# Optimization experiments

Measured on AMD Instinct MI355X. Metric: run time of the kernel, lower is better.

Reference implementation:

```python
import math
import jax, jax.numpy as jnp
import numpy as np

N_HEAD = 16
N_EMBD = 1024
HEAD_DIM = N_EMBD // N_HEAD  # 64
GROUP_SIZE = 64
RESIDUAL_LEN = 32
K_BITS = 2
V_BITS = 2
CLIP = 10000.0


def _fake_quant(x, mn, mx, bits):
    # asymmetric min-max quantize-dequantize with straight-through estimator
    qmax = float(2 ** bits - 1)
    scale = jnp.maximum((mx - mn) / qmax, 1e-8)
    q = jnp.round((x - mn) / scale)
    deq = q * scale + mn
    return x + jax.lax.stop_gradient(deq - x)


def quantize_key(k):
    # per-channel over token groups: [B,H,S,D] -> groups of GROUP_SIZE tokens,
    # min/max over the token axis within each group, per head_dim channel
    B, H, S, D = k.shape
    k = jnp.clip(k, -CLIP, CLIP)
    kg = k.reshape(B, H, S // GROUP_SIZE, GROUP_SIZE, D)
    mn = kg.min(axis=3, keepdims=True)
    mx = kg.max(axis=3, keepdims=True)
    return _fake_quant(kg, mn, mx, K_BITS).reshape(B, H, S, D)


def quantize_value(v):
    # per-token over channel groups: groups of GROUP_SIZE along head_dim
    B, H, S, D = v.shape
    g = GROUP_SIZE if (GROUP_SIZE > 0 and D % GROUP_SIZE == 0) else D
    v = jnp.clip(v, -CLIP, CLIP)
    vg = v.reshape(B, H, S, D // g, g)
    mn = vg.min(axis=-1, keepdims=True)
    mx = vg.max(axis=-1, keepdims=True)
    return _fake_quant(vg, mn, mx, V_BITS).reshape(B, H, S, D)


def setup_inputs() -> dict:
    key = jax.random.key(0)
    ks = jax.random.split(key, 5)
    B, S = 2, 2048
    scale_in = 1.0 / math.sqrt(N_EMBD)
    return {
        "x": jax.random.normal(ks[0], (B, S, N_EMBD), jnp.float32),
        "W_qkv": jax.random.normal(ks[1], (N_EMBD, 3 * N_EMBD), jnp.float32) * scale_in,
        "b_qkv": jax.random.normal(ks[2], (3 * N_EMBD,), jnp.float32) * 0.01,
        "W_proj": jax.random.normal(ks[3], (N_EMBD, N_EMBD), jnp.float32) * scale_in,
        "b_proj": jax.random.normal(ks[4], (N_EMBD,), jnp.float32) * 0.01,
    }


def reference(x, W_qkv, b_qkv, W_proj, b_proj):
    B, S, E = x.shape
    H, D = N_HEAD, HEAD_DIM
    qkv = x @ W_qkv + b_qkv                       # [B,S,3E]
    q, k, v = jnp.split(qkv, 3, axis=-1)
    split = lambda t: t.reshape(B, S, H, D).transpose(0, 2, 1, 3)  # [B,H,S,D]
    q, k, v = split(q), split(k), split(v)

    # KIVI: quantize all keys up to multiple of RESIDUAL_LEN, values except last RESIDUAL_LEN tokens
    if S > RESIDUAL_LEN:
        kql = (S // RESIDUAL_LEN) * RESIDUAL_LEN
        if kql > 0:
            k = jnp.concatenate([quantize_key(k[:, :, :kql]), k[:, :, kql:]], axis=2)
        vql = max(0, S - RESIDUAL_LEN)
        if vql > 0:
            v = jnp.concatenate([quantize_value(v[:, :, :vql]), v[:, :, vql:]], axis=2)

    attn = jnp.einsum("bhqd,bhkd->bhqk", q, k) / math.sqrt(D)
    if S > 1:
        mask = jnp.tril(jnp.ones((S, S), bool))
        attn = jnp.where(mask[None, None], attn, -jnp.inf)
    att = jax.nn.softmax(attn, axis=-1)
    y = jnp.einsum("bhqk,bhkd->bhqd", att, v)     # [B,H,S,D]
    y = y.transpose(0, 2, 1, 3).reshape(B, S, E)
    return y @ W_proj + b_proj
```

## Files before the change

### kernel.cpp

```cpp
#include <hip/hip_runtime.h>
#include <math.h>

#define BATCH 2
#define SEQ   2048
#define NHEAD 16
#define EMB   1024
#define N3E   3072
#define VQL   2016

typedef unsigned short ushort8_t __attribute__((ext_vector_type(8)));
typedef unsigned short ushort4_t __attribute__((ext_vector_type(4)));
typedef short bf16x8 __attribute__((ext_vector_type(8)));
typedef float f32x4 __attribute__((ext_vector_type(4)));
typedef unsigned int uint2_t __attribute__((ext_vector_type(2)));
typedef unsigned int uint4_t __attribute__((ext_vector_type(4)));

__device__ __forceinline__ float clipf(float x) {
    return fminf(fmaxf(x, -10000.0f), 10000.0f);
}
__device__ __forceinline__ float bf2f(unsigned short u) {
    return __uint_as_float(((unsigned)u) << 16);
}
__device__ __forceinline__ unsigned short f2bf(float f) {
    unsigned u = __float_as_uint(f);
    unsigned r = 0x7FFFu + ((u >> 16) & 1u);
    return (unsigned short)((u + r) >> 16);
}
__device__ __forceinline__ unsigned cvtpk(float lo, float hi) {
    unsigned r;
    asm("v_cvt_pk_bf16_f32 %0, %1, %2" : "=v"(r) : "v"(lo), "v"(hi));
    return r;
}

#define QK_PAD 40
__global__ __launch_bounds__(256, 2) void gemm_qkv_mfma(
    const float* __restrict__ X, const float* __restrict__ W,
    const float* __restrict__ bias,
    unsigned short* __restrict__ Qb, unsigned short* __restrict__ Kb,
    unsigned short* __restrict__ Vt)
{
    __shared__ unsigned short A3[3][128][QK_PAD];
    __shared__ unsigned short B3[3][128][QK_PAD];

    const int tid  = threadIdx.x;
    const int wave = tid >> 6, lane = tid & 63, lr = lane & 15, g = lane >> 4;
    const int wr = wave >> 1, wc = wave & 1;
    const int row0 = blockIdx.y * 128, col0 = blockIdx.x * 128;

    const int ra  = tid >> 1,        ca  = (tid & 1) * 16;
    const int cb4 = (tid & 31) * 4,  kb4 = (tid >> 5) * 4;

    const float* gA = X + (size_t)(row0 + ra) * 1024 + ca;
    const float* gB = W + (size_t)kb4 * N3E + col0 + cb4;

    float a_reg[16];
    float b_reg[4][4];

    #pragma unroll
    for (int i = 0; i < 4; ++i) *(float4*)&a_reg[i * 4] = *(const float4*)(gA + i * 4);
    #pragma unroll
    for (int i = 0; i < 4; ++i) *(float4*)b_reg[i] = *(const float4*)(gB + (size_t)i * N3E);

    f32x4 acc[4][4] = {};

    for (int t = 0; t < 32; ++t) {
        __syncthreads();
        unsigned pw[3][8];
        #pragma unroll
        for (int p = 0; p < 8; ++p) {
            float x0 = a_reg[2 * p], x1 = a_reg[2 * p + 1];
            unsigned h = cvtpk(x0, x1);
            float h0 = __uint_as_float(h << 16), h1 = __uint_as_float(h & 0xFFFF0000u);
            float r0 = x0 - h0, r1 = x1 - h1;
            unsigned m = cvtpk(r0, r1);
            float m0 = __uint_as_float(m << 16), m1 = __uint_as_float(m & 0xFFFF0000u);
            unsigned l = cvtpk(r0 - m0, r1 - m1);
            pw[0][p] = h; pw[1][p] = m; pw[2][p] = l;
        }
        #pragma unroll
        for (int term = 0; term < 3; ++term) {
            *(uint4_t*)&A3[term][ra][ca]     = *(uint4_t*)&pw[term][0];
            *(uint4_t*)&A3[term][ra][ca + 8] = *(uint4_t*)&pw[term][4];
        }
        #pragma unroll
        for (int j = 0; j < 4; ++j) {
            unsigned wh[2], wm[2], wl[2];
            #pragma unroll
            for (int ii = 0; ii < 2; ++ii) {
                float x0 = b_reg[2 * ii][j], x1 = b_reg[2 * ii + 1][j];
                unsigned h = cvtpk(x0, x1);
                float h0 = __uint_as_float(h << 16), h1 = __uint_as_float(h & 0xFFFF0000u);
                float r0 = x0 - h0, r1 = x1 - h1;
                unsigned m = cvtpk(r0, r1);
                float m0 = __uint_as_float(m << 16), m1 = __uint_as_float(m & 0xFFFF0000u);
                unsigned l = cvtpk(r0 - m0, r1 - m1);
                wh[ii] = h; wm[ii] = m; wl[ii] = l;
            }
            *(uint2_t*)&B3[0][cb4 + j][kb4] = *(uint2_t*)wh;
            *(uint2_t*)&B3[1][cb4 + j][kb4] = *(uint2_t*)wm;
            *(uint2_t*)&B3[2][cb4 + j][kb4] = *(uint2_t*)wl;
        }
        __syncthreads();

        if (t < 31) {
            #pragma unroll
            for (int i = 0; i < 4; ++i)
                *(float4*)&a_reg[i * 4] = *(const float4*)(gA + (t + 1) * 32 + i * 4);
            #pragma unroll
            for (int i = 0; i < 4; ++i)
                *(float4*)b_reg[i] = *(const float4*)(gB + (size_t)((t + 1) * 32 + i) * N3E);
        }

        bf16x8 af[3][4];
        #pragma unroll
        for (int term = 0; term < 3; ++term)
            #pragma unroll
            for (int m = 0; m < 4; ++m)
                af[term][m] = *(const bf16x8*)&A3[term][wr * 64 + m * 16 + lr][g * 8];
        #pragma unroll
        for (int n = 0; n < 4; ++n) {
            bf16x8 bh = *(const bf16x8*)&B3[0][wc * 64 + n * 16 + lr][g * 8];
            bf16x8 bm = *(const bf16x8*)&B3[1][wc * 64 + n * 16 + lr][g * 8];
            bf16x8 bl = *(const bf16x8*)&B3[2][wc * 64 + n * 16 + lr][g * 8];
            #pragma unroll
            for (int m = 0; m < 4; ++m)
                acc[m][n] = __builtin_amdgcn_mfma_f32_16x16x32_bf16(af[0][m], bh, acc[m][n], 0, 0, 0);
            #pragma unroll
            for (int m = 0; m < 4; ++m)
                acc[m][n] = __builtin_amdgcn_mfma_f32_16x16x32_bf16(af[0][m], bm, acc[m][n], 0, 0, 0);
            #pragma unroll
            for (int m = 0; m < 4; ++m)
                acc[m][n] = __builtin_amdgcn_mfma_f32_16x16x32_bf16(af[1][m], bh, acc[m][n], 0, 0, 0);
            #pragma unroll
            for (int m = 0; m < 4; ++m)
                acc[m][n] = __builtin_amdgcn_mfma_f32_16x16x32_bf16(af[1][m], bm, acc[m][n], 0, 0, 0);
            #pragma unroll
            for (int m = 0; m < 4; ++m)
                acc[m][n] = __builtin_amdgcn_mfma_f32_16x16x32_bf16(af[0][m], bl, acc[m][n], 0, 0, 0);
            #pragma unroll
            for (int m = 0; m < 4; ++m)
                acc[m][n] = __builtin_amdgcn_mfma_f32_16x16x32_bf16(af[2][m], bh, acc[m][n], 0, 0, 0);
        }
    }

    const int which = col0 >> 10;
    const int hcol  = ((col0 + wc * 64) & 1023) >> 6;
    const int b     = row0 >> 11;
    const int s_base = (row0 & 2047) + wr * 64;

    float bo[4];
    #pragma unroll
    for (int n = 0; n < 4; ++n) bo[n] = bias[col0 + wc * 64 + n * 16 + lr];
    #pragma unroll
    for (int m = 0; m < 4; ++m)
        #pragma unroll
        for (int n = 0; n < 4; ++n)
            #pragma unroll
            for (int r = 0; r < 4; ++r)
                acc[m][n][r] += bo[n];

    if (which == 0) {
        unsigned short* qdst = Qb + (((size_t)b * NHEAD + hcol) * SEQ) * 64;
        #pragma unroll
        for (int m = 0; m < 4; ++m)
            #pragma unroll
            for (int r = 0; r < 4; ++r) {
                int s = s_base + m * 16 + g * 4 + r;
                #pragma unroll
                for (int n = 0; n < 4; ++n)
                    qdst[(size_t)s * 64 + n * 16 + lr] = f2bf(acc[m][n][r]);
            }
    } else if (which == 1) {
        #pragma unroll
        for (int n = 0; n < 4; ++n) {
            float cmn = INFINITY, cmx = -INFINITY;
            #pragma unroll
            for (int m = 0; m < 4; ++m)
                #pragma unroll
                for (int r = 0; r < 4; ++r) {
                    float v = clipf(acc[m][n][r]);
                    acc[m][n][r] = v;
                    cmn = fminf(cmn, v); cmx = fmaxf(cmx, v);
                }
            cmn = fminf(cmn, __shfl_xor(cmn, 16)); cmx = fmaxf(cmx, __shfl_xor(cmx, 16));
            cmn = fminf(cmn, __shfl_xor(cmn, 32)); cmx = fmaxf(cmx, __shfl_xor(cmx, 32));
            float scale = fmaxf((cmx - cmn) / 3.0f, 1e-8f);
            #pragma unroll
            for (int m = 0; m < 4; ++m)
                #pragma unroll
                for (int r = 0; r < 4; ++r)
                    acc[m][n][r] = rintf((acc[m][n][r] - cmn) / scale) * scale + cmn;
        }
        unsigned short* kdst = Kb + (((size_t)b * NHEAD + hcol) * SEQ) * 64;
        #pragma unroll
        for (int m = 0; m < 4; ++m)
            #pragma unroll
            for (int r = 0; r < 4; ++r) {
                int s = s_base + m * 16 + g * 4 + r;
                #pragma unroll
                for (int n = 0; n < 4; ++n)
                    kdst[(size_t)s * 64 + n * 16 + lr] = f2bf(acc[m][n][r]);
            }
    } else {
        #pragma unroll
        for (int m = 0; m < 4; ++m)
            #pragma unroll
            for (int r = 0; r < 4; ++r) {
                float c[4];
                #pragma unroll
                for (int n = 0; n < 4; ++n) c[n] = clipf(acc[m][n][r]);
                float mn = fminf(fminf(c[0], c[1]), fminf(c[2], c[3]));
                float mx = fmaxf(fmaxf(c[0], c[1]), fmaxf(c[2], c[3]));
                #pragma unroll
                for (int msk = 1; msk < 16; msk <<= 1) {
                    mn = fminf(mn, __shfl_xor(mn, msk));
                    mx = fmaxf(mx, __shfl_xor(mx, msk));
                }
                int s = s_base + m * 16 + g * 4 + r;
                if (s < VQL) {
                    float scale = fmaxf((mx - mn) / 3.0f, 1e-8f);
                    #pragma unroll
                    for (int n = 0; n < 4; ++n)
                        acc[m][n][r] = rintf((c[n] - mn) / scale) * scale + mn;
                }
            }
        #pragma unroll
        for (int m = 0; m < 4; ++m)
            #pragma unroll
            for (int n = 0; n < 4; ++n) {
                ushort4_t o;
                #pragma unroll
                for (int r = 0; r < 4; ++r) o[r] = f2bf(acc[m][n][r]);
                *(ushort4_t*)(Vt + ((((size_t)b * NHEAD + hcol) * 64) + n * 16 + lr) * SEQ
                                 + s_base + m * 16 + g * 4) = o;
            }
    }
}

__global__ __launch_bounds__(256) void attn_mfma(
    unsigned short* __restrict__ QY,
    const unsigned short* __restrict__ K,
    const unsigned short* __restrict__ Vt)
{
    __shared__ unsigned short Ks [64][72];
    __shared__ unsigned short VsT[64][72];
    __shared__ unsigned short Ps [4][16][72];

    const int tid  = threadIdx.x;
    const int wave = tid >> 6;
    const int lane = tid & 63;
    const int lr   = lane & 15;
    const int g    = lane >> 4;

    const int bid = blockIdx.x;
    const int qt  = 31 - (bid >> 5);
    const int bh  = bid & 31;
    const size_t base = (size_t)bh * (SEQ * 64);

    const int qrow = qt * 64 + wave * 16 + lr;
    const unsigned short* qp = QY + base + (size_t)qrow * 64;
    bf16x8 aq[2];
    #pragma unroll
    for (int ka = 0; ka < 2; ++ka)
        aq[ka] = *(const bf16x8*)(qp + ka * 32 + g * 8);

    f32x4 o[4] = {};
    float m[4]    = {-1e30f, -1e30f, -1e30f, -1e30f};
    float lsum[4] = {};
    const float sc = 0.125f;

    const int str = tid >> 2;
    const int stc = (tid & 3) << 4;

    for (int jt = 0; jt <= qt; ++jt) {
        __syncthreads();
        {
            const unsigned short* kg = K + base + ((size_t)(jt * 64 + str) << 6) + stc;
            *(ushort8_t*)&Ks[str][stc]     = *(const ushort8_t*)kg;
            *(ushort8_t*)&Ks[str][stc + 8] = *(const ushort8_t*)(kg + 8);
            const unsigned short* vg = Vt + base + ((size_t)str << 11) + jt * 64 + stc;
            *(ushort8_t*)&VsT[str][stc]     = *(const ushort8_t*)vg;
            *(ushort8_t*)&VsT[str][stc + 8] = *(const ushort8_t*)(vg + 8);
        }
        __syncthreads();

        f32x4 s[4] = {};
        #pragma unroll
        for (int f = 0; f < 4; ++f) {
            #pragma unroll
            for (int ka = 0; ka < 2; ++ka) {
                bf16x8 bk = *(const bf16x8*)&Ks[f * 16 + lr][ka * 32 + g * 8];
                s[f] = __builtin_amdgcn_mfma_f32_16x16x32_bf16(aq[ka], bk, s[f], 0, 0, 0);
            }
        }

        const bool diag = (jt == qt);
        float mx[4];
        #pragma unroll
        for (int r = 0; r < 4; ++r) {
            const int ql = wave * 16 + g * 4 + r;
            float vmax = -1e30f;
            #pragma unroll
            for (int f = 0; f < 4; ++f) {
                float v = s[f][r] * sc;
                if (diag && (f * 16 + lr) > ql) v = -1e30f;
                s[f][r] = v;
                vmax = fmaxf(vmax, v);
            }
            mx[r] = vmax;
        }
        #pragma unroll
        for (int msk = 1; msk < 16; msk <<= 1)
            #pragma unroll
            for (int r = 0; r < 4; ++r)
                mx[r] = fmaxf(mx[r], __shfl_xor(mx[r], msk));

        float alpha[4], tsum[4];
        #pragma unroll
        for (int r = 0; r < 4; ++r) {
            float mn = fmaxf(m[r], mx[r]);
            alpha[r] = __expf(m[r] - mn);
            m[r] = mn;
            float ts = 0.0f;
            #pragma unroll
            for (int f = 0; f < 4; ++f) {
                float p = __expf(s[f][r] - mn);
                unsigned short ub = f2bf(p);
                Ps[wave][g * 4 + r][f * 16 + lr] = ub;
                ts += bf2f(ub);
            }
            tsum[r] = ts;
        }
        #pragma unroll
        for (int msk = 1; msk < 16; msk <<= 1)
            #pragma unroll
            for (int r = 0; r < 4; ++r)
                tsum[r] += __shfl_xor(tsum[r], msk);
        #pragma unroll
        for (int r = 0; r < 4; ++r) {
            lsum[r] = lsum[r] * alpha[r] + tsum[r];
            #pragma unroll
            for (int df = 0; df < 4; ++df) o[df][r] *= alpha[r];
        }

        asm volatile("s_waitcnt lgkmcnt(0)" ::: "memory");
        __builtin_amdgcn_sched_barrier(0);

        bf16x8 pa[2];
        #pragma unroll
        for (int kb = 0; kb < 2; ++kb)
            pa[kb] = *(const bf16x8*)&Ps[wave][lr][kb * 32 + g * 8];
        #pragma unroll
        for (int df = 0; df < 4; ++df) {
            #pragma unroll
            for (int kb = 0; kb < 2; ++kb) {
                bf16x8 vb = *(const bf16x8*)&VsT[df * 16 + lr][kb * 32 + g * 8];
                o[df] = __builtin_amdgcn_mfma_f32_16x16x32_bf16(pa[kb], vb, o[df], 0, 0, 0);
            }
        }
    }

    float invl[4];
    #pragma unroll
    for (int r = 0; r < 4; ++r) invl[r] = 1.0f / lsum[r];
    #pragma unroll
    for (int df = 0; df < 4; ++df)
        #pragma unroll
        for (int r = 0; r < 4; ++r) {
            int q = qt * 64 + wave * 16 + g * 4 + r;
            QY[base + (size_t)q * 64 + df * 16 + lr] = f2bf(o[df][r] * invl[r]);
        }
}

#define PJ_PAD 72
__global__ __launch_bounds__(256, 2) void gemm_proj_mfma(
    const unsigned short* __restrict__ Y, const float* __restrict__ W,
    const float* __restrict__ bias, float* __restrict__ C)
{
    __shared__ unsigned short A2[2][128][PJ_PAD];
    __shared__ unsigned short B2[2][128][PJ_PAD];

    const int tid  = threadIdx.x;
    const int wave = tid >> 6, lane = tid & 63, lr = lane & 15, g = lane >> 4;
    const int wr = wave >> 1, wc = wave & 1;
    const int row0 = blockIdx.y * 128, col0 = blockIdx.x * 128;
    const int b = row0 >> 11, s0 = row0 & 2047;

    const int ra  = tid >> 1,       ca  = (tid & 1) * 32;
    const int cb4 = (tid & 31) * 4, kb4 = (tid >> 5) * 4;

    ushort8_t a_reg[4];
    float bw[2][4][4];

    {
        const unsigned short* gy = Y + ((((size_t)b * NHEAD + 0) * SEQ + s0 + ra) << 6) + ca;
        #pragma unroll
        for (int i = 0; i < 4; ++i) a_reg[i] = *(const ushort8_t*)(gy + i * 8);
        const float* gw = W + (size_t)kb4 * EMB + col0 + cb4;
        #pragma unroll
        for (int half = 0; half < 2; ++half)
            #pragma unroll
            for (int i = 0; i < 4; ++i)
                *(float4*)bw[half][i] = *(const float4*)(gw + (size_t)(half * 32 + i) * EMB);
        #pragma unroll
        for (int i = 0; i < 4; ++i) *(ushort8_t*)&A2[0][ra][ca + i * 8] = a_reg[i];
        #pragma unroll
        for (int half = 0; half < 2; ++half)
            #pragma unroll
            for (int j = 0; j < 4; ++j) {
                unsigned w2[2];
                w2[0] = cvtpk(bw[half][0][j], bw[half][1][j]);
                w2[1] = cvtpk(bw[half][2][j], bw[half][3][j]);
                *(uint2_t*)&B2[0][cb4 + j][half * 32 + kb4] = *(uint2_t*)w2;
            }
    }
    __syncthreads();

    f32x4 acc[4][4] = {};

    for (int t = 0; t < 16; ++t) {
        const int cur = t & 1;
        if (t < 15) {
            const unsigned short* gy =
                Y + ((((size_t)b * NHEAD + (t + 1)) * SEQ + s0 + ra) << 6) + ca;
            #pragma unroll
            for (int i = 0; i < 4; ++i) a_reg[i] = *(const ushort8_t*)(gy + i * 8);
            const float* gw = W + (size_t)((t + 1) * 64 + kb4) * EMB + col0 + cb4;
            #pragma unroll
            for (int half = 0; half < 2; ++half)
                #pragma unroll
                for (int i = 0; i < 4; ++i)
                    *(float4*)bw[half][i] = *(const float4*)(gw + (size_t)(half * 32 + i) * EMB);
        }
        #pragma unroll
        for (int kk = 0; kk < 2; ++kk) {
            bf16x8 af[4];
            #pragma unroll
            for (int m = 0; m < 4; ++m)
                af[m] = *(const bf16x8*)&A2[cur][wr * 64 + m * 16 + lr][kk * 32 + g * 8];
            #pragma unroll
            for (int n = 0; n < 4; ++n) {
                bf16x8 bf = *(const bf16x8*)&B2[cur][wc * 64 + n * 16 + lr][kk * 32 + g * 8];
                #pragma unroll
                for (int m = 0; m < 4; ++m)
                    acc[m][n] = __builtin_amdgcn_mfma_f32_16x16x32_bf16(af[m], bf, acc[m][n], 0, 0, 0);
            }
        }
        if (t < 15) {
            const int nxt = cur ^ 1;
            #pragma unroll
            for (int i = 0; i < 4; ++i) *(ushort8_t*)&A2[nxt][ra][ca + i * 8] = a_reg[i];
            #pragma unroll
            for (int half = 0; half < 2; ++half)
                #pragma unroll
                for (int j = 0; j < 4; ++j) {
                    unsigned w2[2];
                    w2[0] = cvtpk(bw[half][0][j], bw[half][1][j]);
                    w2[1] = cvtpk(bw[half][2][j], bw[half][3][j]);
                    *(uint2_t*)&B2[nxt][cb4 + j][half * 32 + kb4] = *(uint2_t*)w2;
                }
        }
        __syncthreads();
    }

    float bo[4];
    #pragma unroll
    for (int n = 0; n < 4; ++n) bo[n] = bias[col0 + wc * 64 + n * 16 + lr];
    #pragma unroll
    for (int m = 0; m < 4; ++m)
        #pragma unroll
        for (int r = 0; r < 4; ++r) {
            int mrow = row0 + wr * 64 + m * 16 + g * 4 + r;
            #pragma unroll
            for (int n = 0; n < 4; ++n)
                C[(size_t)mrow * EMB + col0 + wc * 64 + n * 16 + lr] = acc[m][n][r] + bo[n];
        }
}

extern "C" void kernel_launch(void* const* d_in, const int* in_sizes, int n_in,
                              void* d_out, int out_size, void* d_ws, size_t ws_size,
                              hipStream_t stream)
{
    const float* x     = (const float*)d_in[0];
    const float* Wqkv  = (const float*)d_in[1];
    const float* bqkv  = (const float*)d_in[2];
    const float* Wproj = (const float*)d_in[3];
    const float* bproj = (const float*)d_in[4];
    float* out = (float*)d_out;

    const size_t QKV_ELEMS = (size_t)BATCH * NHEAD * SEQ * 64;
    unsigned short* q  = (unsigned short*)d_ws;
    unsigned short* kb = q + QKV_ELEMS;
    unsigned short* vt = kb + QKV_ELEMS;

    gemm_qkv_mfma<<<dim3(N3E / 128, 4096 / 128), 256, 0, stream>>>(x, Wqkv, bqkv, q, kb, vt);
    attn_mfma<<<dim3(32 * 32), 256, 0, stream>>>(q, kb, vt);
    gemm_proj_mfma<<<dim3(EMB / 128, 4096 / 128), 256, 0, stream>>>(q, Wproj, bproj, out);
}
```

Baseline: 310.4 us.

## Pre-split QKV operands to bf16 and repair near-tie quantization values

The fused in-loop fp32-to-3xbf16 splitting in the QKV GEMM is replaced by separate pre-pass kernels that split X into two bf16 terms and transposed W into three. The GEMM then runs three bf16 product passes (hh, hm, mh) instead of six, loading tiles with async global-to-LDS copies into swizzled shared memory. Because the reduced precision can flip K/V quantization rounding near half-integer boundaries, near-tie elements are recorded through an atomic counter. A repair kernel recomputes those elements in higher precision. The cost is extra kernels, workspace traffic, and atomics, and the repair list is capped at a fixed size.

```diff
diff --git a/kernel.cpp b/kernel.cpp
--- a/kernel.cpp
+++ b/kernel.cpp
@@ -7,13 +7,15 @@
 #define EMB   1024
 #define N3E   3072
 #define VQL   2016
+#define REC_CAP 65536
 
 typedef unsigned short ushort8_t __attribute__((ext_vector_type(8)));
 typedef unsigned short ushort4_t __attribute__((ext_vector_type(4)));
 typedef short bf16x8 __attribute__((ext_vector_type(8)));
 typedef float f32x4 __attribute__((ext_vector_type(4)));
 typedef unsigned int uint2_t __attribute__((ext_vector_type(2)));
-typedef unsigned int uint4_t __attribute__((ext_vector_type(4)));
+
+struct __align__(16) Rec { unsigned dst; unsigned mn_pack; float mn; float scale; };
 
 __device__ __forceinline__ float clipf(float x) {
     return fminf(fmaxf(x, -10000.0f), 10000.0f);
@@ -31,115 +33,132 @@
     asm("v_cvt_pk_bf16_f32 %0, %1, %2" : "=v"(r) : "v"(lo), "v"(hi));
     return r;
 }
-
-#define QK_PAD 40
-__global__ __launch_bounds__(256, 2) void gemm_qkv_mfma(
-    const float* __restrict__ X, const float* __restrict__ W,
+__device__ __forceinline__ void async_copy16(const unsigned short* g, unsigned short* lds) {
+    __builtin_amdgcn_global_load_lds(
+        (const __attribute__((address_space(1))) unsigned int*)g,
+        (__attribute__((address_space(3))) unsigned int*)lds, 16, 0, 0);
+}
+
+__global__ __launch_bounds__(256) void split_x_kernel(
+    const float* __restrict__ X,
+    unsigned short* __restrict__ Xh, unsigned short* __restrict__ Xm)
+{
+    const size_t i8 = ((size_t)blockIdx.x * 256 + threadIdx.x) * 8;
+    float4 a = *(const float4*)(X + i8);
+    float4 b = *(const float4*)(X + i8 + 4);
+    float xs[8] = {a.x, a.y, a.z, a.w, b.x, b.y, b.z, b.w};
+    ushort8_t h8, m8;
+    #pragma unroll
+    for (int j = 0; j < 8; ++j) {
+        unsigned short h = f2bf(xs[j]);
+        h8[j] = h;
+        m8[j] = f2bf(xs[j] - bf2f(h));
+    }
+    *(ushort8_t*)(Xh + i8) = h8;
+    *(ushort8_t*)(Xm + i8) = m8;
+}
+
+__global__ __launch_bounds__(256) void split_wt_kernel(
+    const float* __restrict__ W,
+    unsigned short* __restrict__ WTh, unsigned short* __restrict__ WTm,
+    unsigned short* __restrict__ WTl)
+{
+    __shared__ float t[64][65];
+    const int tid = threadIdx.x;
+    const int nt = blockIdx.x * 64, kt = blockIdx.y * 64;
+    const int r = tid >> 2, cg = (tid & 3) * 16;
+    #pragma unroll
+    for (int j = 0; j < 4; ++j) {
+        float4 v = *(const float4*)(W + (size_t)(kt + r) * N3E + nt + cg + j * 4);
+        t[r][cg + j * 4 + 0] = v.x; t[r][cg + j * 4 + 1] = v.y;
+        t[r][cg + j * 4 + 2] = v.z; t[r][cg + j * 4 + 3] = v.w;
+    }
+    __syncthreads();
+    ushort8_t h8[2], m8[2], l8[2];
+    #pragma unroll
+    for (int j = 0; j < 16; ++j) {
+        float v = t[cg + j][r];
+        unsigned short h = f2bf(v);
+        float r1 = v - bf2f(h);
+        unsigned short mm = f2bf(r1);
+        float r2 = r1 - bf2f(mm);
+        h8[j >> 3][j & 7] = h; m8[j >> 3][j & 7] = mm; l8[j >> 3][j & 7] = f2bf(r2);
+    }
+    size_t off = (size_t)(nt + r) * 1024 + kt + cg;
+    *(ushort8_t*)(WTh + off) = h8[0]; *(ushort8_t*)(WTh + off + 8) = h8[1];
+    *(ushort8_t*)(WTm + off) = m8[0]; *(ushort8_t*)(WTm + off + 8) = m8[1];
+    *(ushort8_t*)(WTl + off) = l8[0]; *(ushort8_t*)(WTl + off + 8) = l8[1];
+}
+
+__global__ void zero_cnt_kernel(unsigned* c) {
+    if (threadIdx.x == 0 && blockIdx.x == 0) *c = 0;
+}
+
+__device__ __forceinline__ void push_flag(unsigned* cnt, Rec* recs, unsigned dst,
+                                          int mg, int ng, float mn, float scale) {
+    unsigned idx = atomicAdd(cnt, 1u);
+    if (idx < REC_CAP) {
+        Rec r; r.dst = dst; r.mn_pack = (unsigned)mg | ((unsigned)ng << 12);
+        r.mn = mn; r.scale = scale;
+        recs[idx] = r;
+    }
+}
+
+__global__ __launch_bounds__(256) void gemm_qkv3(
+    const unsigned short* __restrict__ Xh, const unsigned short* __restrict__ Xm,
+    const unsigned short* __restrict__ WTh, const unsigned short* __restrict__ WTm,
     const float* __restrict__ bias,
     unsigned short* __restrict__ Qb, unsigned short* __restrict__ Kb,
-    unsigned short* __restrict__ Vt)
-{
-    __shared__ unsigned short A3[3][128][QK_PAD];
-    __shared__ unsigned short B3[3][128][QK_PAD];
+    unsigned short* __restrict__ Vt,
+    unsigned* __restrict__ cnt, Rec* __restrict__ recs)
+{
+    __shared__ __align__(16) unsigned short As[128 * 64];
+    __shared__ __align__(16) unsigned short Bs[128 * 64];
 
     const int tid  = threadIdx.x;
     const int wave = tid >> 6, lane = tid & 63, lr = lane & 15, g = lane >> 4;
     const int wr = wave >> 1, wc = wave & 1;
     const int row0 = blockIdx.y * 128, col0 = blockIdx.x * 128;
-
-    const int ra  = tid >> 1,        ca  = (tid & 1) * 16;
-    const int cb4 = (tid & 31) * 4,  kb4 = (tid >> 5) * 4;
-
-    const float* gA = X + (size_t)(row0 + ra) * 1024 + ca;
-    const float* gB = W + (size_t)kb4 * N3E + col0 + cb4;
-
-    float a_reg[16];
-    float b_reg[4][4];
-
-    #pragma unroll
-    for (int i = 0; i < 4; ++i) *(float4*)&a_reg[i * 4] = *(const float4*)(gA + i * 4);
-    #pragma unroll
-    for (int i = 0; i < 4; ++i) *(float4*)b_reg[i] = *(const float4*)(gB + (size_t)i * N3E);
+    const int lr7 = lr & 7;
+
+    const int drow = lane >> 3;
+    const int swz8 = ((lane & 7) ^ drow) * 8;
+    const int arow0 = wave * 32;
+
+    const unsigned short* Aseg[3] = {Xh, Xh, Xm};
+    const unsigned short* Bseg[3] = {WTh, WTm, WTh};
 
     f32x4 acc[4][4] = {};
 
-    for (int t = 0; t < 32; ++t) {
-        __syncthreads();
-        unsigned pw[3][8];
-        #pragma unroll
-        for (int p = 0; p < 8; ++p) {
-            float x0 = a_reg[2 * p], x1 = a_reg[2 * p + 1];
-            unsigned h = cvtpk(x0, x1);
-            float h0 = __uint_as_float(h << 16), h1 = __uint_as_float(h & 0xFFFF0000u);
-            float r0 = x0 - h0, r1 = x1 - h1;
-            unsigned m = cvtpk(r0, r1);
-            float m0 = __uint_as_float(m << 16), m1 = __uint_as_float(m & 0xFFFF0000u);
-            unsigned l = cvtpk(r0 - m0, r1 - m1);
-            pw[0][p] = h; pw[1][p] = m; pw[2][p] = l;
-        }
-        #pragma unroll
-        for (int term = 0; term < 3; ++term) {
-            *(uint4_t*)&A3[term][ra][ca]     = *(uint4_t*)&pw[term][0];
-            *(uint4_t*)&A3[term][ra][ca + 8] = *(uint4_t*)&pw[term][4];
-        }
-        #pragma unroll
-        for (int j = 0; j < 4; ++j) {
-            unsigned wh[2], wm[2], wl[2];
-            #pragma unroll
-            for (int ii = 0; ii < 2; ++ii) {
-                float x0 = b_reg[2 * ii][j], x1 = b_reg[2 * ii + 1][j];
-                unsigned h = cvtpk(x0, x1);
-                float h0 = __uint_as_float(h << 16), h1 = __uint_as_float(h & 0xFFFF0000u);
-                float r0 = x0 - h0, r1 = x1 - h1;
-                unsigned m = cvtpk(r0, r1);
-                float m0 = __uint_as_float(m << 16), m1 = __uint_as_float(m & 0xFFFF0000u);
-                unsigned l = cvtpk(r0 - m0, r1 - m1);
-                wh[ii] = h; wm[ii] = m; wl[ii] = l;
-            }
-            *(uint2_t*)&B3[0][cb4 + j][kb4] = *(uint2_t*)wh;
-            *(uint2_t*)&B3[1][cb4 + j][kb4] = *(uint2_t*)wm;
-            *(uint2_t*)&B3[2][cb4 + j][kb4] = *(uint2_t*)wl;
-        }
-        __syncthreads();
-
-        if (t < 31) {
-            #pragma unroll
-            for (int i = 0; i < 4; ++i)
-                *(float4*)&a_reg[i * 4] = *(const float4*)(gA + (t + 1) * 32 + i * 4);
-            #pragma unroll
-            for (int i = 0; i < 4; ++i)
-                *(float4*)b_reg[i] = *(const float4*)(gB + (size_t)((t + 1) * 32 + i) * N3E);
-        }
-
-        bf16x8 af[3][4];
-        #pragma unroll
-        for (int term = 0; term < 3; ++term)
-            #pragma unroll
-            for (int m = 0; m < 4; ++m)
-                af[term][m] = *(const bf16x8*)&A3[term][wr * 64 + m * 16 + lr][g * 8];
-        #pragma unroll
-        for (int n = 0; n < 4; ++n) {
-            bf16x8 bh = *(const bf16x8*)&B3[0][wc * 64 + n * 16 + lr][g * 8];
-            bf16x8 bm = *(const bf16x8*)&B3[1][wc * 64 + n * 16 + lr][g * 8];
-            bf16x8 bl = *(const bf16x8*)&B3[2][wc * 64 + n * 16 + lr][g * 8];
-            #pragma unroll
-            for (int m = 0; m < 4; ++m)
-                acc[m][n] = __builtin_amdgcn_mfma_f32_16x16x32_bf16(af[0][m], bh, acc[m][n], 0, 0, 0);
-            #pragma unroll
-            for (int m = 0; m < 4; ++m)
-                acc[m][n] = __builtin_amdgcn_mfma_f32_16x16x32_bf16(af[0][m], bm, acc[m][n], 0, 0, 0);
-            #pragma unroll
-            for (int m = 0; m < 4; ++m)
-                acc[m][n] = __builtin_amdgcn_mfma_f32_16x16x32_bf16(af[1][m], bh, acc[m][n], 0, 0, 0);
-            #pragma unroll
-            for (int m = 0; m < 4; ++m)
-                acc[m][n] = __builtin_amdgcn_mfma_f32_16x16x32_bf16(af[1][m], bm, acc[m][n], 0, 0, 0);
-            #pragma unroll
-            for (int m = 0; m < 4; ++m)
-                acc[m][n] = __builtin_amdgcn_mfma_f32_16x16x32_bf16(af[0][m], bl, acc[m][n], 0, 0, 0);
-            #pragma unroll
-            for (int m = 0; m < 4; ++m)
-                acc[m][n] = __builtin_amdgcn_mfma_f32_16x16x32_bf16(af[2][m], bh, acc[m][n], 0, 0, 0);
+    for (int seg = 0; seg < 3; ++seg) {
+        const unsigned short* ApL = Aseg[seg] + (size_t)(row0 + arow0 + drow) * 1024 + swz8;
+        const unsigned short* BpL = Bseg[seg] + (size_t)(col0 + arow0 + drow) * 1024 + swz8;
+        for (int tt = 0; tt < 16; ++tt) {
+            __syncthreads();
+            #pragma unroll
+            for (int c = 0; c < 4; ++c) {
+                async_copy16(ApL + (size_t)(c * 8) * 1024 + tt * 64, &As[(arow0 + c * 8) * 64]);
+                async_copy16(BpL + (size_t)(c * 8) * 1024 + tt * 64, &Bs[(arow0 + c * 8) * 64]);
+            }
+            __syncthreads();
+
+            #pragma unroll
+            for (int h = 0; h < 2; ++h) {
+                const int gr = ((h * 4 + g) ^ lr7) * 8;
+                bf16x8 a[4], b[4];
+                #pragma unroll
+                for (int mf = 0; mf < 4; ++mf)
+                    a[mf] = *(const bf16x8*)&As[(wr * 64 + mf * 16 + lr) * 64 + gr];
+                #pragma unroll
+                for (int nf = 0; nf < 4; ++nf)
+                    b[nf] = *(const bf16x8*)&Bs[(wc * 64 + nf * 16 + lr) * 64 + gr];
+                #pragma unroll
+                for (int nf = 0; nf < 4; ++nf)
+                    #pragma unroll
+                    for (int mf = 0; mf < 4; ++mf)
+                        acc[mf][nf] = __builtin_amdgcn_mfma_f32_16x16x32_bf16(
+                            a[mf], b[nf], acc[mf][nf], 0, 0, 0);
+            }
         }
     }
 
@@ -185,11 +204,23 @@
             cmn = fminf(cmn, __shfl_xor(cmn, 16)); cmx = fmaxf(cmx, __shfl_xor(cmx, 16));
             cmn = fminf(cmn, __shfl_xor(cmn, 32)); cmx = fmaxf(cmx, __shfl_xor(cmx, 32));
             float scale = fmaxf((cmx - cmn) / 3.0f, 1e-8f);
+            float tol = 0.5f - 1e-3f / scale;
             #pragma unroll
             for (int m = 0; m < 4; ++m)
                 #pragma unroll
-                for (int r = 0; r < 4; ++r)
-                    acc[m][n][r] = rintf((acc[m][n][r] - cmn) / scale) * scale + cmn;
+                for (int r = 0; r < 4; ++r) {
+                    float f = (acc[m][n][r] - cmn) / scale;
+                    float qv = rintf(f);
+                    if (fabsf(f - qv) > tol) {
+                        int s  = s_base + m * 16 + g * 4 + r;
+                        int mg = row0 + wr * 64 + m * 16 + g * 4 + r;
+                        int ng = col0 + wc * 64 + n * 16 + lr;
+                        unsigned dst = 4194304u +
+                            (unsigned)(((b * NHEAD + hcol) * SEQ + s) * 64 + n * 16 + lr);
+                        push_flag(cnt, recs, dst, mg, ng, cmn, scale);
+                    }
+                    acc[m][n][r] = qv * scale + cmn;
+                }
         }
         unsigned short* kdst = Kb + (((size_t)b * NHEAD + hcol) * SEQ) * 64;
         #pragma unroll
@@ -219,9 +250,20 @@
                 int s = s_base + m * 16 + g * 4 + r;
                 if (s < VQL) {
                     float scale = fmaxf((mx - mn) / 3.0f, 1e-8f);
+                    float tol = 0.5f - 1e-3f / scale;
                     #pragma unroll
-                    for (int n = 0; n < 4; ++n)
-                        acc[m][n][r] = rintf((c[n] - mn) / scale) * scale + mn;
+                    for (int n = 0; n < 4; ++n) {
+                        float f = (c[n] - mn) / scale;
+                        float qv = rintf(f);
+                        if (fabsf(f - qv) > tol) {
+                            int mg = row0 + wr * 64 + m * 16 + g * 4 + r;
+                            int ng = col0 + wc * 64 + n * 16 + lr;
+                            unsigned dst = 8388608u +
+                                (unsigned)((((b * NHEAD + hcol) * 64) + n * 16 + lr) * SEQ + s);
+                            push_flag(cnt, recs, dst, mg, ng, mn, scale);
+                        }
+                        acc[m][n][r] = qv * scale + mn;
+                    }
                 }
             }
         #pragma unroll
@@ -234,6 +276,45 @@
                 *(ushort4_t*)(Vt + ((((size_t)b * NHEAD + hcol) * 64) + n * 16 + lr) * SEQ
                                  + s_base + m * 16 + g * 4) = o;
             }
+    }
+}
+
+__global__ __launch_bounds__(256) void repair_kernel(
+    const float* __restrict__ X,
+    const unsigned short* __restrict__ WTh, const unsigned short* __restrict__ WTm,
+    const unsigned short* __restrict__ WTl,
+    const float* __restrict__ bias, unsigned short* __restrict__ wsu,
+    const unsigned* __restrict__ cnt, const Rec* __restrict__ recs)
+{
+    const int lane = threadIdx.x & 63;
+    const int wid  = blockIdx.x * 4 + (threadIdx.x >> 6);
+    unsigned nrec = *cnt; if (nrec > REC_CAP) nrec = REC_CAP;
+    for (unsigned i = wid; i < nrec; i += gridDim.x * 4) {
+        Rec rc = recs[i];
+        int mg = rc.mn_pack & 4095;
+        int ng = (rc.mn_pack >> 12) & 4095;
+        const float* xr          = X   + (size_t)mg * 1024 + lane * 16;
+        const unsigned short* wh = WTh + (size_t)ng * 1024 + lane * 16;
+        const unsigned short* wm = WTm + (size_t)ng * 1024 + lane * 16;
+        const unsigned short* wl = WTl + (size_t)ng * 1024 + lane * 16;
+        float s = 0.f;
+        #pragma unroll
+        for (int j4 = 0; j4 < 4; ++j4) {
+            float4 xv = *(const float4*)(xr + j4 * 4);
+            float xs[4] = {xv.x, xv.y, xv.z, xv.w};
+            #pragma unroll
+            for (int e = 0; e < 4; ++e) {
+                int j = j4 * 4 + e;
+                s += xs[e] * (bf2f(wh[j]) + bf2f(wm[j]) + bf2f(wl[j]));
+            }
+        }
+        #pragma unroll
+        for (int msk = 1; msk < 64; msk <<= 1) s += __shfl_xor(s, msk);
+        if (lane == 0) {
+            float v = clipf(s + bias[ng]);
+            float val = rintf((v - rc.mn) / rc.scale) * rc.scale + rc.mn;
+            wsu[rc.dst] = f2bf(val);
+        }
     }
 }
 
@@ -488,12 +569,25 @@
     const float* bproj = (const float*)d_in[4];
     float* out = (float*)d_out;
 
-    const size_t QKV_ELEMS = (size_t)BATCH * NHEAD * SEQ * 64;
-    unsigned short* q  = (unsigned short*)d_ws;
-    unsigned short* kb = q + QKV_ELEMS;
-    unsigned short* vt = kb + QKV_ELEMS;
-
-    gemm_qkv_mfma<<<dim3(N3E / 128, 4096 / 128), 256, 0, stream>>>(x, Wqkv, bqkv, q, kb, vt);
+    char* ws = (char*)d_ws;
+    unsigned short* q   = (unsigned short*)ws;
+    unsigned short* kb  = (unsigned short*)(ws + (8u  << 20));
+    unsigned short* vt  = (unsigned short*)(ws + (16u << 20));
+    unsigned short* Xh  = (unsigned short*)(ws + (24u << 20));
+    unsigned short* Xm  = (unsigned short*)(ws + (32u << 20));
+    unsigned short* WTh = (unsigned short*)(ws + (40u << 20));
+    unsigned short* WTm = (unsigned short*)(ws + (46u << 20));
+    unsigned short* WTl = (unsigned short*)(ws + (52u << 20));
+    unsigned*       cnt = (unsigned*)(ws + (58u << 20));
+    Rec*           recs = (Rec*)(ws + (58u << 20) + 256);
+
+    zero_cnt_kernel<<<1, 64, 0, stream>>>(cnt);
+    split_x_kernel<<<2048, 256, 0, stream>>>(x, Xh, Xm);
+    split_wt_kernel<<<dim3(48, 16), 256, 0, stream>>>(Wqkv, WTh, WTm, WTl);
+    gemm_qkv3<<<dim3(N3E / 128, 4096 / 128), 256, 0, stream>>>(
+        Xh, Xm, WTh, WTm, bqkv, q, kb, vt, cnt, recs);
+    repair_kernel<<<128, 256, 0, stream>>>(x, WTh, WTm, WTl, bqkv,
+                                           (unsigned short*)d_ws, cnt, recs);
     attn_mfma<<<dim3(32 * 32), 256, 0, stream>>>(q, kb, vt);
     gemm_proj_mfma<<<dim3(EMB / 128, 4096 / 128), 256, 0, stream>>>(q, Wproj, bproj, out);
 }
```

Measured after the change: 360.8 us. 1.16x slower.
